# Optimization experiments

Hardware: AMD Instinct MI355X
Metric: run time of the kernel (lower is better)

The kernel has to match this reference:

```python
import jax, jax.numpy as jnp
import numpy as np
from jax import lax

BN_EPS = 1e-5

# Straight-through-estimator sign (XNOR-Net BinActive): fwd=sign, bwd=clipped identity
@jax.custom_vjp
def ste_sign(x):
    return jnp.sign(x)

def _ste_fwd(x):
    return jnp.sign(x), x

def _ste_bwd(x, g):
    return (g * (jnp.abs(x) <= 1.0).astype(g.dtype),)

ste_sign.defvjp(_ste_fwd, _ste_bwd)

def conv2d(x, w):
    # x: NCHW, w: OIHW, stride 1, VALID
    return lax.conv_general_dilated(x, w, (1, 1), 'VALID',
                                    dimension_numbers=('NCHW', 'OIHW', 'NCHW'))

def maxpool2(x):
    return lax.reduce_window(x, -jnp.inf, lax.max, (1, 1, 2, 2), (1, 1, 2, 2), 'VALID')

def bn2d(x, gamma, beta):
    # training-mode BatchNorm2d: batch stats over (N,H,W), biased variance
    mean = jnp.mean(x, axis=(0, 2, 3), keepdims=True)
    var = jnp.mean((x - mean) ** 2, axis=(0, 2, 3), keepdims=True)
    xhat = (x - mean) * lax.rsqrt(var + BN_EPS)
    return xhat * gamma[None, :, None, None] + beta[None, :, None, None]

def bn1d(x, gamma, beta):
    mean = jnp.mean(x, axis=0, keepdims=True)
    var = jnp.mean((x - mean) ** 2, axis=0, keepdims=True)
    xhat = (x - mean) * lax.rsqrt(var + BN_EPS)
    return xhat * gamma[None, :] + beta[None, :]

def bin_conv2d(x, w):
    # XNOR-style: binarize input and weight, scale by per-filter alpha = mean|W|
    alpha = jnp.mean(jnp.abs(w), axis=(1, 2, 3))  # [O]
    out = conv2d(ste_sign(x), ste_sign(w))
    return out * alpha[None, :, None, None]

def bin_linear(x, w):
    # w: [out_features, in_features]
    alpha = jnp.mean(jnp.abs(w), axis=1)  # [out_features]
    return (ste_sign(x) @ ste_sign(w).T) * alpha[None, :]


def setup_inputs() -> dict:
    key = jax.random.key(0)
    ks = jax.random.split(key, 8)
    B = 8192
    inp = {
        'x': jax.random.normal(ks[0], (B, 1, 28, 28), dtype=jnp.float32),
        'conv1_w': jax.random.normal(ks[1], (20, 1, 5, 5), dtype=jnp.float32) * 0.2,
        'bn1_g': jnp.ones((20,), jnp.float32),
        'bn1_b': jnp.zeros((20,), jnp.float32),
        'conv2_w': jax.random.normal(ks[2], (50, 20, 5, 5), dtype=jnp.float32) * 0.04,
        'bn2_g': jnp.ones((50,), jnp.float32),
        'bn2_b': jnp.zeros((50,), jnp.float32),
        'fc1_w': jax.random.normal(ks[3], (500, 800), dtype=jnp.float32) * 0.035,
        'bn3_g': jnp.ones((500,), jnp.float32),
        'bn3_b': jnp.zeros((500,), jnp.float32),
        'fc2_w': jax.random.normal(ks[4], (10, 500), dtype=jnp.float32) * 0.045,
        'fc2_b': jnp.zeros((10,), jnp.float32),
    }
    return inp


def reference(x, conv1_w, bn1_g, bn1_b, conv2_w, bn2_g, bn2_b,
              fc1_w, bn3_g, bn3_b, fc2_w, fc2_b):
    h = conv2d(x, conv1_w)                 # [B,20,24,24]
    h = jax.nn.relu(bn2d(h, bn1_g, bn1_b))
    h = maxpool2(h)                        # [B,20,12,12]
    h = bin_conv2d(h, conv2_w)             # [B,50,8,8]
    h = jax.nn.relu(bn2d(h, bn2_g, bn2_b))
    h = maxpool2(h)                        # [B,50,4,4]
    h = h.reshape(-1, 50 * 4 * 4)          # [B,800]
    h = bin_linear(h, fc1_w)               # [B,500]
    h = jax.nn.relu(bn1d(h, bn3_g, bn3_b))
    return h @ fc2_w.T + fc2_b[None, :]    # [B,10]
```

## Files before the change

kernel.cpp:

```cpp
#include <hip/hip_runtime.h>
#include <stdint.h>

#define BATCH 8192
#define NJOB  1179648

__global__ __launch_bounds__(256) void k_pack(const float* __restrict__ w2,
    const float* __restrict__ w3, unsigned* __restrict__ wpos2,
    unsigned* __restrict__ wneg2, float* __restrict__ alpha2,
    unsigned* __restrict__ wpos3, unsigned* __restrict__ wneg3,
    float* __restrict__ alpha3, int* __restrict__ flags2, int* __restrict__ flags3){
  __shared__ int zf;
  int tid = threadIdx.x;
  if (tid == 0) zf = 0;
  __syncthreads();
  if (blockIdx.x < 5){
    int t = blockIdx.x*256 + tid;
    int had0 = 0;
    if (t < 1250){
      int o = t/25, k = t%25;
      unsigned p=0, n=0;
      for (int i=0;i<20;i++){
        float v = w2[(o*20+i)*25 + k];
        if (v > 0.f) p |= 1u<<i;
        else if (v < 0.f) n |= 1u<<i;
        else had0 = 1;
      }
      wpos2[t] = p; wneg2[t] = n;
    }
    if (t < 50){
      float s = 0.f;
      for (int i=0;i<500;i++) s += fabsf(w2[t*500+i]);
      alpha2[t] = s / 500.f;
    }
    if (had0) atomicOr(&zf, 1);
    __syncthreads();
    if (tid == 0) flags2[blockIdx.x] = zf;
  } else {
    int t = (blockIdx.x-5)*256 + tid;
    int had0 = 0;
    if (t < 12500){
      int j = t/25, w = t%25;
      unsigned p=0, n=0;
      for (int bb=0;bb<32;bb++){
        float v = w3[j*800 + w*32 + bb];
        if (v > 0.f) p |= 1u<<bb;
        else if (v < 0.f) n |= 1u<<bb;
        else had0 = 1;
      }
      wpos3[t] = p; wneg3[t] = n;
    }
    if (t < 500){
      float s = 0.f;
      for (int i=0;i<800;i++) s += fabsf(w3[t*800+i]);
      alpha3[t] = s / 800.f;
    }
    if (had0) atomicOr(&zf, 1);
    __syncthreads();
    if (tid == 0) flags3[blockIdx.x-5] = zf;
  }
}


#define CONV1_ROWS(IPTR)                                                      \
  float vA0=0.f,vA1=0.f,vA2=0.f,vA3=0.f;                                      \
  float vB0=0.f,vB1=0.f,vB2=0.f,vB3=0.f;                                      \
  _Pragma("unroll")                                                           \
  for (int r=0;r<6;r++){                                                      \
    const float2* rp = (const float2*)((IPTR) + r*28);                        \
    float2 p0 = rp[0], p1 = rp[1], p2 = rp[2];                                \
    float row0=p0.x, row1=p0.y, row2=p1.x, row3=p1.y, row4=p2.x, row5=p2.y;   \
    if (r<5){                                                                 \
      _Pragma("unroll")                                                       \
      for (int kx=0;kx<5;kx++){                                               \
        float e0 = (kx==0?row0:kx==1?row1:kx==2?row2:kx==3?row3:row4);        \
        float e1 = (kx==0?row1:kx==1?row2:kx==2?row3:kx==3?row4:row5);        \
        float w = wa[r*5+kx], u = wb[r*5+kx];                                 \
        vA0=fmaf(e0,w,vA0); vA1=fmaf(e1,w,vA1);                               \
        vB0=fmaf(e0,u,vB0); vB1=fmaf(e1,u,vB1);                               \
      }                                                                       \
    }                                                                         \
    if (r>0){                                                                 \
      _Pragma("unroll")                                                       \
      for (int kx=0;kx<5;kx++){                                               \
        float e0 = (kx==0?row0:kx==1?row1:kx==2?row2:kx==3?row3:row4);        \
        float e1 = (kx==0?row1:kx==1?row2:kx==2?row3:kx==3?row4:row5);        \
        float w = wa[(r-1)*5+kx], u = wb[(r-1)*5+kx];                         \
        vA2=fmaf(e0,w,vA2); vA3=fmaf(e1,w,vA3);                               \
        vB2=fmaf(e0,u,vB2); vB3=fmaf(e1,u,vB3);                               \
      }                                                                       \
    }                                                                         \
  }

template<bool STORE_MM>
__global__ __launch_bounds__(256) void k_conv1_stats(const float* __restrict__ x,
        const float* __restrict__ w1, const float* __restrict__ g1,
        float* __restrict__ part1, float2* __restrict__ c1ext){
  __shared__ float img[8*784];
  __shared__ float red[4][40];
  int tid = threadIdx.x;
  size_t base = (size_t)blockIdx.x * 8;
  const float4* xv = (const float4*)(x + base*784);
  float4* iv = (float4*)img;
  for (int i=tid;i<1568;i+=256) iv[i] = xv[i];
  __syncthreads();
  int lane = tid & 63, wid = tid >> 6;
#pragma unroll 1
  for (int cg=0; cg<10; ++cg){
    float wa[25], wb[25];
#pragma unroll
    for (int k=0;k<25;k++){ wa[k]=w1[(2*cg)*25+k]; wb[k]=w1[(2*cg+1)*25+k]; }
    float gA = g1[2*cg], gB = g1[2*cg+1];
    float sa=0.f, qa=0.f, sb=0.f, qb=0.f;
#pragma unroll 1
    for (int job=tid; job<8*144; job+=256){
      int li = job/144, pp = job%144;
      int py = pp/12, px = pp%12;
      const float* ip = &img[li*784 + py*56 + px*2];
      CONV1_ROWS(ip)
      sa += (vA0+vA1)+(vA2+vA3);
      qa = fmaf(vA0,vA0, fmaf(vA1,vA1, fmaf(vA2,vA2, fmaf(vA3,vA3, qa))));
      sb += (vB0+vB1)+(vB2+vB3);
      qb = fmaf(vB0,vB0, fmaf(vB1,vB1, fmaf(vB2,vB2, fmaf(vB3,vB3, qb))));
      if (STORE_MM){
        float mxA = fmaxf(fmaxf(vA0,vA1),fmaxf(vA2,vA3));
        float mnA = fminf(fminf(vA0,vA1),fminf(vA2,vA3));
        float mxB = fmaxf(fmaxf(vB0,vB1),fmaxf(vB2,vB3));
        float mnB = fminf(fminf(vB0,vB1),fminf(vB2,vB3));
        float eA = (gA > 0.f) ? mxA : mnA;
        float eB = (gB > 0.f) ? mxB : mnB;
        c1ext[(size_t)cg*NJOB + (base+li)*144 + pp] = make_float2(eA,eB);
      }
    }
#pragma unroll
    for (int d=32; d>0; d>>=1){
      sa += __shfl_down(sa,d); qa += __shfl_down(qa,d);
      sb += __shfl_down(sb,d); qb += __shfl_down(qb,d);
    }
    if (lane==0){
      red[wid][(2*cg)*2]   = sa; red[wid][(2*cg)*2+1]   = qa;
      red[wid][(2*cg+1)*2] = sb; red[wid][(2*cg+1)*2+1] = qb;
    }
  }
  __syncthreads();
  if (tid < 40)
    part1[blockIdx.x*40 + tid] = red[0][tid]+red[1][tid]+red[2][tid]+red[3][tid];
}

__global__ __launch_bounds__(256) void k_reduce1(const float* __restrict__ part1,
        const float* __restrict__ g, const float* __restrict__ b,
        float* __restrict__ s1t1){
  __shared__ double rs[256], rq[256];
  int c = blockIdx.x;
  int tid = threadIdx.x;
  double s=0.0, q=0.0;
  for (int i=tid;i<1024;i+=256){
    s += (double)part1[i*40 + c*2];
    q += (double)part1[i*40 + c*2 + 1];
  }
  rs[tid]=s; rq[tid]=q;
  __syncthreads();
  for (int d=128; d>0; d>>=1){
    if (tid<d){ rs[tid]+=rs[tid+d]; rq[tid]+=rq[tid+d]; }
    __syncthreads();
  }
  if (tid==0){
    double N = 8192.0*576.0;
    double mean = rs[0]/N, var = rq[0]/N - mean*mean;
    double r = 1.0/sqrt(var + 1e-5);
    double sc = (double)g[c]*r;
    s1t1[c*2]   = (float)sc;
    s1t1[c*2+1] = (float)((double)b[c] - mean*sc);
  }
}

__global__ __launch_bounds__(256) void k_conv1_bin(const float* __restrict__ x,
        const float* __restrict__ w1, const float* __restrict__ s1t1,
        unsigned* __restrict__ mask1){
  __shared__ float img[8*784];
  __shared__ float st[40];
  __shared__ unsigned lw[8*144];
  int tid = threadIdx.x;
  size_t base = (size_t)blockIdx.x * 8;
  const float4* xv = (const float4*)(x + base*784);
  float4* iv = (float4*)img;
  for (int i=tid;i<1568;i+=256) iv[i] = xv[i];
  for (int i=tid;i<8*144;i+=256) lw[i] = 0u;
  if (tid < 40) st[tid] = s1t1[tid];
  __syncthreads();
#pragma unroll 1
  for (int cg=0; cg<10; ++cg){
    float wa[25], wb[25];
#pragma unroll
    for (int k=0;k<25;k++){ wa[k]=w1[(2*cg)*25+k]; wb[k]=w1[(2*cg+1)*25+k]; }
    float sA = st[(2*cg)*2],   tA = st[(2*cg)*2+1];
    float sB = st[(2*cg+1)*2], tB = st[(2*cg+1)*2+1];
#pragma unroll 1
    for (int job=tid; job<8*144; job+=256){
      int li = job/144, pp = job%144;
      int py = pp/12, px = pp%12;
      const float* ip = &img[li*784 + py*56 + px*2];
      CONV1_ROWS(ip)
      unsigned bA = (fmaf(vA0,sA,tA) > 0.f) || (fmaf(vA1,sA,tA) > 0.f) ||
                    (fmaf(vA2,sA,tA) > 0.f) || (fmaf(vA3,sA,tA) > 0.f);
      unsigned bB = (fmaf(vB0,sB,tB) > 0.f) || (fmaf(vB1,sB,tB) > 0.f) ||
                    (fmaf(vB2,sB,tB) > 0.f) || (fmaf(vB3,sB,tB) > 0.f);
      lw[job] |= (bA << (2*cg)) | (bB << (2*cg+1));
    }
  }
  __syncthreads();
  for (int i=tid;i<8*144;i+=256){
    int li = i/144, pp = i%144;
    mask1[(base+li)*144 + pp] = lw[i];
  }
}

__global__ __launch_bounds__(256) void k_conv2f(const float2* __restrict__ c1ext,
    const float* __restrict__ s1t1, const unsigned* __restrict__ wpos,
    const unsigned* __restrict__ wneg, const int* __restrict__ flags2,
    short* __restrict__ S16){
  __shared__ unsigned m1[4*144];
  __shared__ float st[40];
  int tid = threadIdx.x;
  size_t base = (size_t)blockIdx.x * 4;
  bool slow = (flags2[0]|flags2[1]|flags2[2]|flags2[3]|flags2[4]) != 0;
  if (tid < 40) st[tid] = s1t1[tid];
  __syncthreads();
  for (int job=tid; job<4*144; job+=256){
    int li = job/144, pp = job%144;
    unsigned word = 0;
#pragma unroll
    for (int cg=0; cg<10; ++cg){
      float2 v = c1ext[(size_t)cg*NJOB + (base+li)*144 + pp];
      word |= ((fmaf(v.x, st[4*cg+0], st[4*cg+1]) > 0.f) ? 1u : 0u) << (2*cg);
      word |= ((fmaf(v.y, st[4*cg+2], st[4*cg+3]) > 0.f) ? 1u : 0u) << (2*cg+1);
    }
    m1[job] = word;
  }
  __syncthreads();
  int lane = tid & 63, wid = tid >> 6;
  int y2 = lane >> 3, x2 = lane & 7;
  unsigned mw[25];
  const unsigned* mrow = &m1[wid*144];
#pragma unroll
  for (int ky=0;ky<5;ky++)
#pragma unroll
    for (int kx=0;kx<5;kx++)
      mw[ky*5+kx] = mrow[(y2+ky)*12 + x2+kx];
  short* sp = &S16[((base+wid)*50)*64 + lane];
  if (!slow){
    int pbase = 0;
#pragma unroll
    for (int k=0;k<25;k++) pbase += __popc(mw[k]);
#pragma unroll 1
    for (int o=0;o<50;o++){
      const unsigned* n = &wneg[o*25];
      int Sn=0;
#pragma unroll
      for (int k=0;k<25;k++) Sn += __popc(mw[k] & n[k]);
      sp[o*64] = (short)(pbase - 2*Sn);
    }
  } else {
#pragma unroll 1
    for (int o=0;o<50;o++){
      const unsigned* p = &wpos[o*25];
      const unsigned* n = &wneg[o*25];
      int S=0;
#pragma unroll
      for (int k=0;k<25;k++){
        unsigned m = mw[k];
        S += __popc(m & p[k]) - __popc(m & n[k]);
      }
      sp[o*64] = (short)S;
    }
  }
}

__global__ __launch_bounds__(256) void k_conv2(const unsigned* __restrict__ mask1,
    const unsigned* __restrict__ wpos, const unsigned* __restrict__ wneg,
    const int* __restrict__ flags2, short* __restrict__ S16){
  __shared__ unsigned m1[4*144];
  int tid = threadIdx.x;
  size_t base = (size_t)blockIdx.x * 4;
  bool slow = (flags2[0]|flags2[1]|flags2[2]|flags2[3]|flags2[4]) != 0;
  for (int i=tid;i<4*144;i+=256) m1[i] = mask1[base*144 + i];
  __syncthreads();
  int lane = tid & 63, wid = tid >> 6;
  int y2 = lane >> 3, x2 = lane & 7;
  unsigned mw[25];
  const unsigned* mrow = &m1[wid*144];
#pragma unroll
  for (int ky=0;ky<5;ky++)
#pragma unroll
    for (int kx=0;kx<5;kx++)
      mw[ky*5+kx] = mrow[(y2+ky)*12 + x2+kx];
  short* sp = &S16[((base+wid)*50)*64 + lane];
  if (!slow){
    int pbase = 0;
#pragma unroll
    for (int k=0;k<25;k++) pbase += __popc(mw[k]);
#pragma unroll 1
    for (int o=0;o<50;o++){
      const unsigned* n = &wneg[o*25];
      int Sn=0;
#pragma unroll
      for (int k=0;k<25;k++) Sn += __popc(mw[k] & n[k]);
      sp[o*64] = (short)(pbase - 2*Sn);
    }
  } else {
#pragma unroll 1
    for (int o=0;o<50;o++){
      const unsigned* p = &wpos[o*25];
      const unsigned* n = &wneg[o*25];
      int S=0;
#pragma unroll
      for (int k=0;k<25;k++){
        unsigned m = mw[k];
        S += __popc(m & p[k]) - __popc(m & n[k]);
      }
      sp[o*64] = (short)S;
    }
  }
}

__global__ __launch_bounds__(256) void k_stats2(const short* __restrict__ S16,
        int* __restrict__ part2){
  int tid = threadIdx.x;
  int lane = tid & 63, wid = tid >> 6;
  const short* p = S16 + (size_t)blockIdx.x * 32 * 3200;
  int rs[13], rq[13];
#pragma unroll
  for (int k=0;k<13;k++){ rs[k]=0; rq[k]=0; }
#pragma unroll 1
  for (int im=0; im<32; ++im){
    const short* q = p + im*3200 + tid;
#pragma unroll
    for (int k=0;k<13;k++){
      if (wid + 4*k < 50){
        int v = q[256*k];
        rs[k] += v; rq[k] += v*v;
      }
    }
  }
#pragma unroll
  for (int k=0;k<13;k++){
    int o = wid + 4*k;
    if (o < 50){
      int s = rs[k], q2 = rq[k];
#pragma unroll
      for (int d=32; d>0; d>>=1){ s += __shfl_down(s,d); q2 += __shfl_down(q2,d); }
      if (lane==0){
        part2[blockIdx.x*100 + o*2]     = s;
        part2[blockIdx.x*100 + o*2 + 1] = q2;
      }
    }
  }
}

__global__ __launch_bounds__(256) void k_reduce2(const int* __restrict__ part2,
        int nchunk, const float* __restrict__ alpha2, const float* __restrict__ g,
        const float* __restrict__ b, float* __restrict__ s2t2){
  __shared__ long long rs[256], rq[256];
  int o = blockIdx.x;
  int tid = threadIdx.x;
  long long s=0, q=0;
  for (int i=tid;i<nchunk;i+=256){
    s += part2[i*100 + o*2];
    q += part2[i*100 + o*2 + 1];
  }
  rs[tid]=s; rq[tid]=q;
  __syncthreads();
  for (int d=128; d>0; d>>=1){
    if (tid<d){ rs[tid]+=rs[tid+d]; rq[tid]+=rq[tid+d]; }
    __syncthreads();
  }
  if (tid==0){
    double N = 8192.0*64.0;
    double meanS = (double)rs[0]/N, E2 = (double)rq[0]/N;
    double varS = E2 - meanS*meanS;
    double a = (double)alpha2[o];
    double mean_g = a*meanS, var_g = a*a*varS;
    double r = 1.0/sqrt(var_g + 1e-5);
    double sc = (double)g[o]*r;
    s2t2[o*2]   = (float)(sc*a);
    s2t2[o*2+1] = (float)((double)b[o] - mean_g*sc);
  }
}

#define BIN2_POOL_BODY                                                        \
    unsigned long long bal = __ballot(cond);                                  \
    unsigned long long t4 = bal | (bal>>1) | (bal>>8) | (bal>>9);             \
    bool pb = (lane < 16) && ((t4 >> (16*(lane>>2) + 2*(lane&3))) & 1ull);    \
    unsigned long long bal2 = __ballot(pb);                                   \
    if (lane==0){                                                             \
      unsigned pooled16 = (unsigned)(bal2 & 0xFFFFull);                       \
      lw[wid*25 + (o>>1)] |= pooled16 << (16*(o&1));                          \
    }

__global__ __launch_bounds__(256) void k_bin2_lite(const short* __restrict__ S16,
    const float* __restrict__ s2t2, unsigned* __restrict__ mask2){
  __shared__ float st[100];
  __shared__ unsigned lw[100];
  int tid = threadIdx.x;
  if (tid < 100){ st[tid] = s2t2[tid]; lw[tid] = 0u; }
  __syncthreads();
  int lane = tid & 63, wid = tid >> 6;
  size_t img = (size_t)blockIdx.x*4 + wid;
#pragma unroll 1
  for (int o=0;o<50;o++){
    int S = S16[(img*50 + o)*64 + lane];
    bool cond = fmaf((float)S, st[o*2], st[o*2+1]) > 0.f;
    BIN2_POOL_BODY
  }
  __syncthreads();
  if (tid < 100) mask2[blockIdx.x*100 + tid] = lw[tid];
}

__global__ __launch_bounds__(256) void k_fc1(const unsigned* __restrict__ mask2,
    const unsigned* __restrict__ wpos, const unsigned* __restrict__ wneg,
    const int* __restrict__ flags3, short* __restrict__ S3){
  __shared__ unsigned m2s[8*25];
  __shared__ short s3s[8*500];
  int tid = threadIdx.x;
  size_t base = (size_t)blockIdx.x * 8;
  for (int i=tid;i<200;i+=256) m2s[i] = mask2[base*25 + i];
  __syncthreads();
  int f = 0;
  for (int i=0;i<49;i++) f |= flags3[i];
  int bl = tid & 7;
  int jg = tid >> 3;
  const unsigned* mrow = &m2s[bl*25];
  if (f == 0){
    int pbase = 0;
#pragma unroll
    for (int w=0;w<25;w++) pbase += __popc(mrow[w]);
#pragma unroll 1
    for (int j=jg; j<500; j+=32){
      const unsigned* n = &wneg[j*25];
      int Sn = 0;
#pragma unroll
      for (int w=0;w<25;w++) Sn += __popc(mrow[w] & n[w]);
      s3s[bl*500 + j] = (short)(pbase - 2*Sn);
    }
  } else {
#pragma unroll 1
    for (int j=jg; j<500; j+=32){
      const unsigned* p = &wpos[j*25];
      const unsigned* n = &wneg[j*25];
      int S = 0;
#pragma unroll
      for (int w=0;w<25;w++){
        unsigned m = mrow[w];
        S += __popc(m & p[w]) - __popc(m & n[w]);
      }
      s3s[bl*500 + j] = (short)S;
    }
  }
  __syncthreads();
  for (int i=tid;i<8*500;i+=256) S3[base*500 + i] = s3s[i];
}

__global__ __launch_bounds__(256) void k_stats3(const short* __restrict__ S3,
                                                int* __restrict__ part3){
  int tid = threadIdx.x;
  const short* p = &S3[(size_t)blockIdx.x * 64 * 500];
  int s0=0,q0=0,s1=0,q1=0;
  for (int b=0;b<64;b++){
    int v0 = p[b*500 + tid];
    s0 += v0; q0 += v0*v0;
    if (tid < 244){
      int v1 = p[b*500 + tid + 256];
      s1 += v1; q1 += v1*v1;
    }
  }
  part3[blockIdx.x*1000 + tid*2]     = s0;
  part3[blockIdx.x*1000 + tid*2 + 1] = q0;
  if (tid < 244){
    part3[blockIdx.x*1000 + (tid+256)*2]     = s1;
    part3[blockIdx.x*1000 + (tid+256)*2 + 1] = q1;
  }
}

__global__ __launch_bounds__(256) void k_reduce3(const int* __restrict__ part3,
        int nchunk, const float* __restrict__ alpha3, const float* __restrict__ g,
        const float* __restrict__ b, float* __restrict__ s3t3){
  __shared__ long long rs[256], rq[256];
  int j = blockIdx.x;
  int tid = threadIdx.x;
  long long s=0, q=0;
  for (int i=tid;i<nchunk;i+=256){
    s += part3[i*1000 + j*2];
    q += part3[i*1000 + j*2 + 1];
  }
  rs[tid]=s; rq[tid]=q;
  __syncthreads();
  for (int d=128; d>0; d>>=1){
    if (tid<d){ rs[tid]+=rs[tid+d]; rq[tid]+=rq[tid+d]; }
    __syncthreads();
  }
  if (tid==0){
    double N = 8192.0;
    double meanS = (double)rs[0]/N, E2 = (double)rq[0]/N;
    double varS = E2 - meanS*meanS;
    double a = (double)alpha3[j];
    double mean_u = a*meanS, var_u = a*a*varS;
    double r = 1.0/sqrt(var_u + 1e-5);
    double sc = (double)g[j]*r;
    s3t3[j*2]   = (float)(sc*a);
    s3t3[j*2+1] = (float)((double)b[j] - mean_u*sc);
  }
}

__global__ __launch_bounds__(256) void k_final(const short* __restrict__ S3,
    const float* __restrict__ s3t3, const float* __restrict__ fc2w,
    const float* __restrict__ fc2b, float* __restrict__ out){
  __shared__ float w[5000];
  __shared__ float st[1000];
  __shared__ float bias[10];
  int tid = threadIdx.x;
  for (int i=tid;i<5000;i+=256) w[i] = fc2w[i];
  for (int i=tid;i<1000;i+=256) st[i] = s3t3[i];
  if (tid<10) bias[tid] = fc2b[tid];
  __syncthreads();
  int sub = tid & 7;
  int li  = tid >> 3;
  size_t b = (size_t)blockIdx.x*32 + li;
  const short* sp = &S3[b*500];
  float acc[10];
#pragma unroll
  for (int m=0;m<10;m++) acc[m] = 0.f;
#pragma unroll 1
  for (int j=sub; j<500; j+=8){
    float h = fmaf((float)sp[j], st[j*2], st[j*2+1]);
    h = fmaxf(h, 0.f);
#pragma unroll
    for (int m=0;m<10;m++) acc[m] = fmaf(h, w[m*500+j], acc[m]);
  }
#pragma unroll
  for (int m=0;m<10;m++){
    float v = acc[m];
    v += __shfl_xor(v, 1);
    v += __shfl_xor(v, 2);
    v += __shfl_xor(v, 4);
    acc[m] = v;
  }
  if (sub == 0){
#pragma unroll
    for (int m=0;m<10;m++) out[b*10 + m] = acc[m] + bias[m];
  }
}

extern "C" void kernel_launch(void* const* d_in, const int* in_sizes, int n_in,
                              void* d_out, int out_size, void* d_ws, size_t ws_size,
                              hipStream_t stream){
  const float* x    = (const float*)d_in[0];
  const float* w1   = (const float*)d_in[1];
  const float* bn1g = (const float*)d_in[2];
  const float* bn1b = (const float*)d_in[3];
  const float* w2   = (const float*)d_in[4];
  const float* bn2g = (const float*)d_in[5];
  const float* bn2b = (const float*)d_in[6];
  const float* w3   = (const float*)d_in[7];
  const float* bn3g = (const float*)d_in[8];
  const float* bn3b = (const float*)d_in[9];
  const float* w4   = (const float*)d_in[10];
  const float* b4   = (const float*)d_in[11];
  float* out = (float*)d_out;
  (void)in_sizes; (void)n_in; (void)out_size;

  char* wsb = (char*)d_ws;
  size_t off = 0;
  auto alloc = [&](size_t n){ size_t o = off; off = (off + n + 255) & ~(size_t)255; return o; };
  float*    s1t1   = (float*)(wsb + alloc(40*sizeof(float)));
  float*    s2t2   = (float*)(wsb + alloc(100*sizeof(float)));
  float*    s3t3   = (float*)(wsb + alloc(1000*sizeof(float)));
  float*    alpha2 = (float*)(wsb + alloc(50*sizeof(float)));
  float*    alpha3 = (float*)(wsb + alloc(500*sizeof(float)));
  int*      flags2 = (int*)(wsb + alloc(5*4));
  int*      flags3 = (int*)(wsb + alloc(49*4));
  unsigned* wpos2  = (unsigned*)(wsb + alloc(1250*4));
  unsigned* wneg2  = (unsigned*)(wsb + alloc(1250*4));
  unsigned* wpos3  = (unsigned*)(wsb + alloc(12500*4));
  unsigned* wneg3  = (unsigned*)(wsb + alloc(12500*4));
  float*    part1  = (float*)(wsb + alloc(1024*40*4));
  int*      part2  = (int*)(wsb + alloc(2048*100*4));
  int*      part3  = (int*)(wsb + alloc(128*1000*4));
  unsigned* mask1  = (unsigned*)(wsb + alloc((size_t)BATCH*144*4));
  unsigned* mask2  = (unsigned*)(wsb + alloc((size_t)BATCH*25*4));
  short*    S3     = (short*)(wsb + alloc((size_t)BATCH*500*2));
  short*    S16    = (short*)(wsb + alloc((size_t)BATCH*50*64*2));
  bool useS16 = (ws_size >= off);
  float2*   c1ext  = (float2*)(wsb + alloc((size_t)10*NJOB*8));
  bool useMM  = (ws_size >= off);

  hipLaunchKernelGGL(k_pack, dim3(54), dim3(256), 0, stream,
                     w2, w3, wpos2, wneg2, alpha2, wpos3, wneg3, alpha3, flags2, flags3);
  if (useMM)
    hipLaunchKernelGGL(HIP_KERNEL_NAME(k_conv1_stats<true>),  dim3(1024), dim3(256), 0, stream, x, w1, bn1g, part1, c1ext);
  else
    hipLaunchKernelGGL(HIP_KERNEL_NAME(k_conv1_stats<false>), dim3(1024), dim3(256), 0, stream, x, w1, bn1g, part1, c1ext);
  hipLaunchKernelGGL(k_reduce1,      dim3(20),    dim3(256), 0, stream, part1, bn1g, bn1b, s1t1);

  if (useMM && useS16){
    hipLaunchKernelGGL(k_conv2f,     dim3(2048),  dim3(256), 0, stream, c1ext, s1t1, wpos2, wneg2, flags2, S16);
  } else {
    hipLaunchKernelGGL(k_conv1_bin,  dim3(1024),  dim3(256), 0, stream, x, w1, s1t1, mask1);
    hipLaunchKernelGGL(k_conv2,      dim3(2048),  dim3(256), 0, stream, mask1, wpos2, wneg2, flags2, S16);
  }
  hipLaunchKernelGGL(k_stats2,       dim3(256),   dim3(256), 0, stream, S16, part2);
  hipLaunchKernelGGL(k_reduce2,      dim3(50),    dim3(256), 0, stream, part2, 256, alpha2, bn2g, bn2b, s2t2);
  hipLaunchKernelGGL(k_bin2_lite,    dim3(2048),  dim3(256), 0, stream, S16, s2t2, mask2);
  hipLaunchKernelGGL(k_fc1,          dim3(1024),  dim3(256), 0, stream, mask2, wpos3, wneg3, flags3, S3);
  hipLaunchKernelGGL(k_stats3,       dim3(128),   dim3(256), 0, stream, S3, part3);
  hipLaunchKernelGGL(k_reduce3,      dim3(500),   dim3(256), 0, stream, part3, 128, alpha3, bn3g, bn3b, s3t3);
  hipLaunchKernelGGL(k_final,        dim3(256),   dim3(256), 0, stream, S3, s3t3, w4, b4, out);
}
```

Measured before the change: 309.3 us.

## Swap conv1 stats loop order to load each input patch once for all channels

The conv1 statistics kernel now loops over pixel jobs on the outside and all 10 channel pairs on the inside. The 6x6 input patch is read from shared memory once into registers and reused for all 20 output channels, instead of being re-read for each channel group. Per-channel sums and squares are kept in 40 register accumulators and reduced once at the end. Weights are now read from global/constant memory inside the fully unrolled loop, and a launch-bounds occupancy hint is added. Register pressure rises, which risks spills or lower occupancy.

New measurement: 324.2 us. +4.8%, slower.

```diff
diff --git a/kernel.cpp b/kernel.cpp
--- a/kernel.cpp
+++ b/kernel.cpp
@@ -60,6 +60,107 @@
   }
 }
 
+
+#define PE(r,c) (((c)&1) ? a2[(r)*3+((c)>>1)].y : a2[(r)*3+((c)>>1)].x)
+
+template<bool STORE_MM>
+__global__ __launch_bounds__(256, 4) void k_conv1_stats(const float* __restrict__ x,
+        const float* __restrict__ w1, const float* __restrict__ g1,
+        float* __restrict__ part1, float2* __restrict__ c1ext){
+  __shared__ float img[8*784];
+  __shared__ float red[4][40];
+  int tid = threadIdx.x;
+  size_t base = (size_t)blockIdx.x * 8;
+  const float4* xv = (const float4*)(x + base*784);
+  float4* iv = (float4*)img;
+  for (int i=tid;i<1568;i+=256) iv[i] = xv[i];
+  __syncthreads();
+  int lane = tid & 63, wid = tid >> 6;
+  float sum[20], sq[20];
+#pragma unroll
+  for (int c=0;c<20;c++){ sum[c]=0.f; sq[c]=0.f; }
+#pragma unroll 1
+  for (int job=tid; job<8*144; job+=256){
+    int li = job/144, pp = job%144;
+    int py = pp/12, px = pp%12;
+    const float* ip = &img[li*784 + py*56 + px*2];
+    float2 a2[18];
+#pragma unroll
+    for (int r=0;r<6;r++){
+      const float2* rp = (const float2*)(ip + r*28);
+      a2[r*3+0]=rp[0]; a2[r*3+1]=rp[1]; a2[r*3+2]=rp[2];
+    }
+    size_t J = (base+li)*144 + pp;
+#pragma unroll
+    for (int cg=0; cg<10; ++cg){
+      float vA0=0.f,vA1=0.f,vA2=0.f,vA3=0.f;
+      float vB0=0.f,vB1=0.f,vB2=0.f,vB3=0.f;
+#pragma unroll
+      for (int ky=0;ky<5;ky++)
+#pragma unroll
+        for (int kx=0;kx<5;kx++){
+          float w = w1[(2*cg)*25 + ky*5+kx];
+          float u = w1[(2*cg+1)*25 + ky*5+kx];
+          float e00=PE(ky,kx), e01=PE(ky,kx+1);
+          float e10=PE(ky+1,kx), e11=PE(ky+1,kx+1);
+          vA0=fmaf(e00,w,vA0); vA1=fmaf(e01,w,vA1);
+          vA2=fmaf(e10,w,vA2); vA3=fmaf(e11,w,vA3);
+          vB0=fmaf(e00,u,vB0); vB1=fmaf(e01,u,vB1);
+          vB2=fmaf(e10,u,vB2); vB3=fmaf(e11,u,vB3);
+        }
+      sum[2*cg]   += (vA0+vA1)+(vA2+vA3);
+      sq[2*cg]     = fmaf(vA0,vA0, fmaf(vA1,vA1, fmaf(vA2,vA2, fmaf(vA3,vA3, sq[2*cg]))));
+      sum[2*cg+1] += (vB0+vB1)+(vB2+vB3);
+      sq[2*cg+1]   = fmaf(vB0,vB0, fmaf(vB1,vB1, fmaf(vB2,vB2, fmaf(vB3,vB3, sq[2*cg+1]))));
+      if (STORE_MM){
+        float mxA = fmaxf(fmaxf(vA0,vA1),fmaxf(vA2,vA3));
+        float mnA = fminf(fminf(vA0,vA1),fminf(vA2,vA3));
+        float mxB = fmaxf(fmaxf(vB0,vB1),fmaxf(vB2,vB3));
+        float mnB = fminf(fminf(vB0,vB1),fminf(vB2,vB3));
+        float eA = (g1[2*cg]   > 0.f) ? mxA : mnA;
+        float eB = (g1[2*cg+1] > 0.f) ? mxB : mnB;
+        c1ext[(size_t)cg*NJOB + J] = make_float2(eA,eB);
+      }
+    }
+  }
+#pragma unroll
+  for (int c=0;c<20;c++){
+    float v1=sum[c], v2=sq[c];
+#pragma unroll
+    for (int d=32; d>0; d>>=1){ v1 += __shfl_down(v1,d); v2 += __shfl_down(v2,d); }
+    if (lane==0){ red[wid][c*2]=v1; red[wid][c*2+1]=v2; }
+  }
+  __syncthreads();
+  if (tid < 40)
+    part1[blockIdx.x*40 + tid] = red[0][tid]+red[1][tid]+red[2][tid]+red[3][tid];
+}
+
+__global__ __launch_bounds__(256) void k_reduce1(const float* __restrict__ part1,
+        const float* __restrict__ g, const float* __restrict__ b,
+        float* __restrict__ s1t1){
+  __shared__ double rs[256], rq[256];
+  int c = blockIdx.x;
+  int tid = threadIdx.x;
+  double s=0.0, q=0.0;
+  for (int i=tid;i<1024;i+=256){
+    s += (double)part1[i*40 + c*2];
+    q += (double)part1[i*40 + c*2 + 1];
+  }
+  rs[tid]=s; rq[tid]=q;
+  __syncthreads();
+  for (int d=128; d>0; d>>=1){
+    if (tid<d){ rs[tid]+=rs[tid+d]; rq[tid]+=rq[tid+d]; }
+    __syncthreads();
+  }
+  if (tid==0){
+    double N = 8192.0*576.0;
+    double mean = rs[0]/N, var = rq[0]/N - mean*mean;
+    double r = 1.0/sqrt(var + 1e-5);
+    double sc = (double)g[c]*r;
+    s1t1[c*2]   = (float)sc;
+    s1t1[c*2+1] = (float)((double)b[c] - mean*sc);
+  }
+}
 
 #define CONV1_ROWS(IPTR)                                                      \
   float vA0=0.f,vA1=0.f,vA2=0.f,vA3=0.f;                                      \
@@ -91,88 +192,6 @@
     }                                                                         \
   }
 
-template<bool STORE_MM>
-__global__ __launch_bounds__(256) void k_conv1_stats(const float* __restrict__ x,
-        const float* __restrict__ w1, const float* __restrict__ g1,
-        float* __restrict__ part1, float2* __restrict__ c1ext){
-  __shared__ float img[8*784];
-  __shared__ float red[4][40];
-  int tid = threadIdx.x;
-  size_t base = (size_t)blockIdx.x * 8;
-  const float4* xv = (const float4*)(x + base*784);
-  float4* iv = (float4*)img;
-  for (int i=tid;i<1568;i+=256) iv[i] = xv[i];
-  __syncthreads();
-  int lane = tid & 63, wid = tid >> 6;
-#pragma unroll 1
-  for (int cg=0; cg<10; ++cg){
-    float wa[25], wb[25];
-#pragma unroll
-    for (int k=0;k<25;k++){ wa[k]=w1[(2*cg)*25+k]; wb[k]=w1[(2*cg+1)*25+k]; }
-    float gA = g1[2*cg], gB = g1[2*cg+1];
-    float sa=0.f, qa=0.f, sb=0.f, qb=0.f;
-#pragma unroll 1
-    for (int job=tid; job<8*144; job+=256){
-      int li = job/144, pp = job%144;
-      int py = pp/12, px = pp%12;
-      const float* ip = &img[li*784 + py*56 + px*2];
-      CONV1_ROWS(ip)
-      sa += (vA0+vA1)+(vA2+vA3);
-      qa = fmaf(vA0,vA0, fmaf(vA1,vA1, fmaf(vA2,vA2, fmaf(vA3,vA3, qa))));
-      sb += (vB0+vB1)+(vB2+vB3);
-      qb = fmaf(vB0,vB0, fmaf(vB1,vB1, fmaf(vB2,vB2, fmaf(vB3,vB3, qb))));
-      if (STORE_MM){
-        float mxA = fmaxf(fmaxf(vA0,vA1),fmaxf(vA2,vA3));
-        float mnA = fminf(fminf(vA0,vA1),fminf(vA2,vA3));
-        float mxB = fmaxf(fmaxf(vB0,vB1),fmaxf(vB2,vB3));
-        float mnB = fminf(fminf(vB0,vB1),fminf(vB2,vB3));
-        float eA = (gA > 0.f) ? mxA : mnA;
-        float eB = (gB > 0.f) ? mxB : mnB;
-        c1ext[(size_t)cg*NJOB + (base+li)*144 + pp] = make_float2(eA,eB);
-      }
-    }
-#pragma unroll
-    for (int d=32; d>0; d>>=1){
-      sa += __shfl_down(sa,d); qa += __shfl_down(qa,d);
-      sb += __shfl_down(sb,d); qb += __shfl_down(qb,d);
-    }
-    if (lane==0){
-      red[wid][(2*cg)*2]   = sa; red[wid][(2*cg)*2+1]   = qa;
-      red[wid][(2*cg+1)*2] = sb; red[wid][(2*cg+1)*2+1] = qb;
-    }
-  }
-  __syncthreads();
-  if (tid < 40)
-    part1[blockIdx.x*40 + tid] = red[0][tid]+red[1][tid]+red[2][tid]+red[3][tid];
-}
-
-__global__ __launch_bounds__(256) void k_reduce1(const float* __restrict__ part1,
-        const float* __restrict__ g, const float* __restrict__ b,
-        float* __restrict__ s1t1){
-  __shared__ double rs[256], rq[256];
-  int c = blockIdx.x;
-  int tid = threadIdx.x;
-  double s=0.0, q=0.0;
-  for (int i=tid;i<1024;i+=256){
-    s += (double)part1[i*40 + c*2];
-    q += (double)part1[i*40 + c*2 + 1];
-  }
-  rs[tid]=s; rq[tid]=q;
-  __syncthreads();
-  for (int d=128; d>0; d>>=1){
-    if (tid<d){ rs[tid]+=rs[tid+d]; rq[tid]+=rq[tid+d]; }
-    __syncthreads();
-  }
-  if (tid==0){
-    double N = 8192.0*576.0;
-    double mean = rs[0]/N, var = rq[0]/N - mean*mean;
-    double r = 1.0/sqrt(var + 1e-5);
-    double sc = (double)g[c]*r;
-    s1t1[c*2]   = (float)sc;
-    s1t1[c*2+1] = (float)((double)b[c] - mean*sc);
-  }
-}
-
 __global__ __launch_bounds__(256) void k_conv1_bin(const float* __restrict__ x,
         const float* __restrict__ w1, const float* __restrict__ s1t1,
         unsigned* __restrict__ mask1){
```
